# Performance work log

Hardware: AMD Instinct MI355X
Metric: run time of the kernel (lower is better)

Reference implementation:

```python
import jax, jax.numpy as jnp
import numpy as np

N_HEAD = 16
SIZE_PER_HEAD = 64
NEG_BIG = 1e12


def _len_mask(lengths, T):
    # Faithful to: mask = 1 - cumsum(one_hot(len, T), 1)
    # -> 1.0 for positions < len, 0.0 for positions >= len (all ones if len == T).
    pos = jnp.arange(T)
    return (pos[None, :] < lengths[:, 0, None]).astype(jnp.float32)  # [B, T]


def setup_inputs() -> dict:
    key = jax.random.key(0)
    ks = jax.random.split(key, 8)
    B, T, D = 2, 2048, 1024
    Q_seq = jax.random.normal(ks[0], (B, T, D), dtype=jnp.float32)
    K_seq = jax.random.normal(ks[1], (B, T, D), dtype=jnp.float32)
    V_seq = jax.random.normal(ks[2], (B, T, D), dtype=jnp.float32)
    Q_len = jax.random.randint(ks[3], (B, 1), 0, T, dtype=jnp.int32)
    V_len = jax.random.randint(ks[4], (B, 1), 0, T, dtype=jnp.int32)
    s = 1.0 / np.sqrt(D)
    WQ = jax.random.normal(ks[5], (D, N_HEAD * SIZE_PER_HEAD), dtype=jnp.float32) * s
    WK = jax.random.normal(ks[6], (D, N_HEAD * SIZE_PER_HEAD), dtype=jnp.float32) * s
    WV = jax.random.normal(ks[7], (D, N_HEAD * SIZE_PER_HEAD), dtype=jnp.float32) * s
    return {"Q_seq": Q_seq, "K_seq": K_seq, "V_seq": V_seq,
            "Q_len": Q_len, "V_len": V_len, "WQ": WQ, "WK": WK, "WV": WV}


def reference(Q_seq, K_seq, V_seq, Q_len, V_len, WQ, WK, WV):
    B, Tq, _ = Q_seq.shape
    Tk = K_seq.shape[1]
    H, dh = N_HEAD, SIZE_PER_HEAD

    q = (Q_seq @ WQ).reshape(B, Tq, H, dh)  # [B,Tq,H,dh]
    k = (K_seq @ WK).reshape(B, Tk, H, dh)
    v = (V_seq @ WV).reshape(B, Tk, H, dh)

    # scaled dot-product scores [B,H,Tq,Tk]
    A = jnp.einsum('bqhd,bkhd->bhqk', q, k) / np.sqrt(dh).astype(np.float32)

    # additive key-length mask over the key axis (original: permute+mask+permute)
    kmask = _len_mask(V_len, Tk)  # [B,Tk]
    A = A - (1.0 - kmask)[:, None, None, :] * NEG_BIG
    A = jax.nn.softmax(A, axis=-1)

    O = jnp.einsum('bhqk,bkhd->bqhd', A, v).reshape(B, Tq, H * dh)

    # multiplicative query-length mask
    qmask = _len_mask(Q_len, Tq)  # [B,Tq]
    return O * qmask[:, :, None]
```

## Files before the change

kernel.cpp:

```cpp
#include <hip/hip_runtime.h>


using short8   = __attribute__((ext_vector_type(8))) short;
using floatx4  = __attribute__((ext_vector_type(4))) float;
using floatx16 = __attribute__((ext_vector_type(16))) float;
using uintx4   = __attribute__((ext_vector_type(4))) unsigned int;
using ushort4v = __attribute__((ext_vector_type(4))) unsigned short;

__device__ __forceinline__ unsigned short f2bf(float f) {
    unsigned int u = __builtin_bit_cast(unsigned int, f);
    u += 0x7fffu + ((u >> 16) & 1u);
    return (unsigned short)(u >> 16);
}

__global__ __launch_bounds__(256) void cvt_kernel(
    const float* __restrict__ Qs, const float* __restrict__ Ks,
    const float* __restrict__ Vs, const int* __restrict__ Qlen,
    const int* __restrict__ Vlen, unsigned short* __restrict__ abf)
{
    int z = blockIdx.y, row = blockIdx.x;
    int b = row >> 11, rib = row & 2047;
    int ql = Qlen[b]; int vl = Vlen[b]; int vle = vl ? vl : 2048;
    int lim = (z == 0) ? ((ql + 127) & ~127) : ((vle + 127) & ~127);
    if (rib >= lim) return;
    const float* src = (z == 0) ? Qs : ((z == 1) ? Ks : Vs);
    int t = threadIdx.x;
    float4 v = *reinterpret_cast<const float4*>(src + (size_t)row * 1024 + t * 4);
    ushort4v o;
    o[0] = f2bf(v.x); o[1] = f2bf(v.y); o[2] = f2bf(v.z); o[3] = f2bf(v.w);
    *reinterpret_cast<ushort4v*>(abf + (size_t)z * 4194304u + (size_t)row * 1024 + t * 4) = o;
}

__global__ __launch_bounds__(256) void wt_kernel(
    const float* __restrict__ W0, const float* __restrict__ W1,
    const float* __restrict__ W2, unsigned short* __restrict__ out)
{
    __shared__ float tile[64][65];
    int z = blockIdx.z;
    const float* W = (z == 0) ? W0 : ((z == 1) ? W1 : W2);
    unsigned short* O = out + (size_t)z * 1048576u;
    int r0 = blockIdx.y * 64, c0 = blockIdx.x * 64;
    int t = threadIdx.x;
#pragma unroll
    for (int i = 0; i < 16; i++) {
        int idx = t + i * 256; int r = idx >> 6, c = idx & 63;
        tile[r][c] = W[(size_t)(r0 + r) * 1024 + c0 + c];
    }
    __syncthreads();
#pragma unroll
    for (int i = 0; i < 16; i++) {
        int idx = t + i * 256; int c = idx >> 6, r = idx & 63;
        O[(size_t)(c0 + c) * 1024 + r0 + r] = f2bf(tile[r][c]);
    }
}

template <bool PRECVT>
__global__ __launch_bounds__(256) void proj_kernel(
    const float* __restrict__ Qs, const float* __restrict__ Ks,
    const float* __restrict__ Vs, const unsigned short* __restrict__ abf,
    const unsigned short* __restrict__ wt,
    const int* __restrict__ Qlen, const int* __restrict__ Vlen,
    unsigned short* __restrict__ q, unsigned short* __restrict__ k,
    unsigned short* __restrict__ vT)
{
    __shared__ alignas(16) unsigned short As[128][72];
    __shared__ alignas(16) unsigned short Bs[128][72];

    int z = blockIdx.z;
    int tid = threadIdx.x;
    int m0 = blockIdx.y * 128, n0 = blockIdx.x * 128;
    int b = m0 >> 11, rib = m0 & 2047;
    int ql = Qlen[b]; int vl = Vlen[b]; int vle = vl ? vl : 2048;
    int lim = (z == 0) ? ((ql + 127) & ~127) : ((vle + 127) & ~127);
    if (rib >= lim) return;

    const float* Af = (z == 0) ? Qs : ((z == 1) ? Ks : Vs);
    const unsigned short* Ab = abf + (size_t)z * 4194304u;
    const unsigned short* Bt = wt + (size_t)z * 1048576u;

    int w = tid >> 6, lane = tid & 63, g = lane >> 4, lr = lane & 15;
    int wr = w >> 1, wc = w & 1;

    floatx4 acc[4][4];
#pragma unroll
    for (int m = 0; m < 4; m++)
#pragma unroll
        for (int n = 0; n < 4; n++) {
#pragma unroll
            for (int r = 0; r < 4; r++) acc[m][n][r] = 0.f;
        }

    int srow = tid >> 1, scol = (tid & 1) * 32;

    short8 pa[4], pb[4];
    float4 fa[8];

    if constexpr (PRECVT) {
#pragma unroll
        for (int i = 0; i < 4; i++)
            pa[i] = *reinterpret_cast<const short8*>(Ab + (size_t)(m0 + srow) * 1024 + scol + i * 8);
    } else {
#pragma unroll
        for (int i = 0; i < 8; i++)
            fa[i] = *reinterpret_cast<const float4*>(Af + (size_t)(m0 + srow) * 1024 + scol + i * 4);
    }
#pragma unroll
    for (int i = 0; i < 4; i++)
        pb[i] = *reinterpret_cast<const short8*>(Bt + (size_t)(n0 + srow) * 1024 + scol + i * 8);

    for (int kb = 0; kb < 1024; kb += 64) {
        __syncthreads();
        if constexpr (PRECVT) {
#pragma unroll
            for (int i = 0; i < 4; i++)
                *reinterpret_cast<short8*>(&As[srow][scol + i * 8]) = pa[i];
        } else {
#pragma unroll
            for (int i = 0; i < 4; i++) {
                short8 h;
                h[0] = (short)f2bf(fa[2*i].x);   h[1] = (short)f2bf(fa[2*i].y);
                h[2] = (short)f2bf(fa[2*i].z);   h[3] = (short)f2bf(fa[2*i].w);
                h[4] = (short)f2bf(fa[2*i+1].x); h[5] = (short)f2bf(fa[2*i+1].y);
                h[6] = (short)f2bf(fa[2*i+1].z); h[7] = (short)f2bf(fa[2*i+1].w);
                *reinterpret_cast<short8*>(&As[srow][scol + i * 8]) = h;
            }
        }
#pragma unroll
        for (int i = 0; i < 4; i++)
            *reinterpret_cast<short8*>(&Bs[srow][scol + i * 8]) = pb[i];
        __syncthreads();

        if (kb + 64 < 1024) {
            if constexpr (PRECVT) {
#pragma unroll
                for (int i = 0; i < 4; i++)
                    pa[i] = *reinterpret_cast<const short8*>(Ab + (size_t)(m0 + srow) * 1024 + kb + 64 + scol + i * 8);
            } else {
#pragma unroll
                for (int i = 0; i < 8; i++)
                    fa[i] = *reinterpret_cast<const float4*>(Af + (size_t)(m0 + srow) * 1024 + kb + 64 + scol + i * 4);
            }
#pragma unroll
            for (int i = 0; i < 4; i++)
                pb[i] = *reinterpret_cast<const short8*>(Bt + (size_t)(n0 + srow) * 1024 + kb + 64 + scol + i * 8);
        }

#pragma unroll
        for (int kc = 0; kc < 2; kc++) {
            short8 af[4], bf[4];
#pragma unroll
            for (int m = 0; m < 4; m++)
                af[m] = *reinterpret_cast<const short8*>(&As[wr * 64 + m * 16 + lr][kc * 32 + g * 8]);
#pragma unroll
            for (int n = 0; n < 4; n++)
                bf[n] = *reinterpret_cast<const short8*>(&Bs[wc * 64 + n * 16 + lr][kc * 32 + g * 8]);
#pragma unroll
            for (int m = 0; m < 4; m++)
#pragma unroll
                for (int n = 0; n < 4; n++)
                    acc[m][n] = __builtin_amdgcn_mfma_f32_16x16x32_bf16(af[m], bf[n], acc[m][n], 0, 0, 0);
        }
    }

    if (z < 2) {
        unsigned short* outp = (z == 0) ? q : k;
#pragma unroll
        for (int m = 0; m < 4; m++) {
            int row0 = m0 + wr * 64 + m * 16 + g * 4;
#pragma unroll
            for (int n = 0; n < 4; n++) {
                int col = n0 + wc * 64 + n * 16 + lr;
#pragma unroll
                for (int r = 0; r < 4; r++)
                    outp[(size_t)(row0 + r) * 1024 + col] = f2bf(acc[m][n][r]);
            }
        }
    } else {
#pragma unroll
        for (int m = 0; m < 4; m++) {
            int row0 = m0 + wr * 64 + m * 16 + g * 4;
            int bb = row0 >> 11, t0 = row0 & 2047;
#pragma unroll
            for (int n = 0; n < 4; n++) {
                int col = n0 + wc * 64 + n * 16 + lr;
                ushort4v pk;
#pragma unroll
                for (int r = 0; r < 4; r++) pk[r] = f2bf(acc[m][n][r]);
                *reinterpret_cast<ushort4v*>(vT + (size_t)(bb * 1024 + col) * 2048 + t0) = pk;
            }
        }
    }
}

__global__ __launch_bounds__(128, 2) void attn_kernel(
    const unsigned short* __restrict__ q, const unsigned short* __restrict__ k,
    const unsigned short* __restrict__ vT, const int* __restrict__ Qlen,
    const int* __restrict__ Vlen, float* __restrict__ out)
{
    __shared__ alignas(16) unsigned short ks[64][72];
    __shared__ alignas(16) unsigned short vs[64][72];

    int tid = threadIdx.x;
    int w = tid >> 6, lane = tid & 63;
    int j = lane & 31, hi = lane >> 5;

    int blk = blockIdx.x, xcd = blk & 7, idx = blk >> 3;
    int bh = xcd * 4 + (idx >> 5), qtile = idx & 31;
    int b = bh >> 4, h = bh & 15;
    int qlen = Qlen[b]; int vl = Vlen[b]; int vle = vl ? vl : 2048;
    int qrow0 = qtile * 64 + w * 32;

    if (qtile * 64 >= qlen) {
        int zr = qtile * 64 + (tid >> 1);
        float* p = out + (size_t)(b * 2048 + zr) * 1024 + h * 64 + (tid & 1) * 32;
        float4 z4; z4.x = 0.f; z4.y = 0.f; z4.z = 0.f; z4.w = 0.f;
#pragma unroll
        for (int s = 0; s < 8; s++) reinterpret_cast<float4*>(p)[s] = z4;
        return;
    }

    short8 qf[4];
    {
        const unsigned short* qp = q + (size_t)(b * 2048 + qrow0 + j) * 1024 + h * 64 + hi * 8;
#pragma unroll
        for (int c = 0; c < 4; c++) qf[c] = *reinterpret_cast<const short8*>(qp + c * 16);
    }

    floatx16 O0, O1;
#pragma unroll
    for (int t = 0; t < 16; t++) { O0[t] = 0.f; O1[t] = 0.f; }
    float m_r = -3.0e38f, l_r = 0.f;

    int nt = (vle + 63) >> 6;

    int srow = tid >> 1, scol = (tid & 1) * 32;
    const unsigned short* kg = k + (size_t)(b * 2048 + srow) * 1024 + h * 64 + scol;
    const unsigned short* vg = vT + (size_t)(b * 1024 + h * 64 + srow) * 2048 + scol;
    short8 pk[4], pv[4];
#pragma unroll
    for (int i = 0; i < 4; i++) {
        pk[i] = *reinterpret_cast<const short8*>(kg + i * 8);
        pv[i] = *reinterpret_cast<const short8*>(vg + i * 8);
    }

    const float CEXP = 0.18033688011112042f;

    for (int it = 0; it < nt; ++it) {
        int kt = it * 64;
        __syncthreads();
#pragma unroll
        for (int i = 0; i < 4; i++) {
            *reinterpret_cast<short8*>(&ks[srow][scol + i * 8]) = pk[i];
            *reinterpret_cast<short8*>(&vs[srow][scol + i * 8]) = pv[i];
        }
        __syncthreads();
        if (it + 1 < nt) {
            const unsigned short* kg2 = kg + (size_t)(kt + 64) * 1024;
            const unsigned short* vg2 = vg + (kt + 64);
#pragma unroll
            for (int i = 0; i < 4; i++) {
                pk[i] = *reinterpret_cast<const short8*>(kg2 + i * 8);
                pv[i] = *reinterpret_cast<const short8*>(vg2 + i * 8);
            }
        }

        floatx16 s0, s1;
#pragma unroll
        for (int t = 0; t < 16; t++) { s0[t] = 0.f; s1[t] = 0.f; }
        {
            short8 kf0[4], kf1[4];
#pragma unroll
            for (int c = 0; c < 4; c++) {
                kf0[c] = *reinterpret_cast<const short8*>(&ks[j][c * 16 + hi * 8]);
                kf1[c] = *reinterpret_cast<const short8*>(&ks[32 + j][c * 16 + hi * 8]);
            }
#pragma unroll
            for (int c = 0; c < 4; c++) {
                s0 = __builtin_amdgcn_mfma_f32_32x32x16_bf16(kf0[c], qf[c], s0, 0, 0, 0);
                s1 = __builtin_amdgcn_mfma_f32_32x32x16_bf16(kf1[c], qf[c], s1, 0, 0, 0);
            }
        }

        if (kt + 64 > vle) {
#pragma unroll
            for (int t = 0; t < 16; t++) {
                int kl = (t & 3) + 8 * (t >> 2) + 4 * hi;
                if (kt + kl >= vle)      s0[t] = -8.0e12f;
                if (kt + 32 + kl >= vle) s1[t] = -8.0e12f;
            }
        }

        float mx = s0[0];
#pragma unroll
        for (int t = 1; t < 16; t++) mx = fmaxf(mx, s0[t]);
#pragma unroll
        for (int t = 0; t < 16; t++) mx = fmaxf(mx, s1[t]);
        float lm = fmaxf(mx, __shfl_xor(mx, 32));

        if (__any(lm > m_r + 64.f)) {
            float mn = fmaxf(m_r, lm);
            float al = __builtin_amdgcn_exp2f((m_r - mn) * CEXP);
            m_r = mn;
            l_r *= al;
#pragma unroll
            for (int t = 0; t < 16; t++) { O0[t] *= al; O1[t] *= al; }
        }
        float nm = -m_r * CEXP;
#pragma unroll
        for (int t = 0; t < 16; t++) {
            s0[t] = __builtin_amdgcn_exp2f(fmaf(s0[t], CEXP, nm));
            s1[t] = __builtin_amdgcn_exp2f(fmaf(s1[t], CEXP, nm));
        }
        float rs = 0.f;
#pragma unroll
        for (int t = 0; t < 16; t++) rs += s0[t] + s1[t];
        l_r += rs;

        unsigned int pbw[4][4];
        {
            unsigned int D[4][2];
#pragma unroll
            for (int s = 0; s < 4; s++) {
                asm("v_cvt_pk_bf16_f32 %0, %1, %2" : "=v"(D[s][0]) : "v"(s0[4*s+0]), "v"(s0[4*s+1]));
                asm("v_cvt_pk_bf16_f32 %0, %1, %2" : "=v"(D[s][1]) : "v"(s0[4*s+2]), "v"(s0[4*s+3]));
            }
#pragma unroll
            for (int u = 0; u < 2; u++) {
                asm volatile("v_permlane32_swap_b32 %0, %1" : "+v"(D[0][u]), "+v"(D[1][u]));
                asm volatile("v_permlane32_swap_b32 %0, %1" : "+v"(D[2][u]), "+v"(D[3][u]));
                pbw[0][u] = D[0][u]; pbw[0][u + 2] = D[1][u];
                pbw[1][u] = D[2][u]; pbw[1][u + 2] = D[3][u];
            }
#pragma unroll
            for (int s = 0; s < 4; s++) {
                asm("v_cvt_pk_bf16_f32 %0, %1, %2" : "=v"(D[s][0]) : "v"(s1[4*s+0]), "v"(s1[4*s+1]));
                asm("v_cvt_pk_bf16_f32 %0, %1, %2" : "=v"(D[s][1]) : "v"(s1[4*s+2]), "v"(s1[4*s+3]));
            }
#pragma unroll
            for (int u = 0; u < 2; u++) {
                asm volatile("v_permlane32_swap_b32 %0, %1" : "+v"(D[0][u]), "+v"(D[1][u]));
                asm volatile("v_permlane32_swap_b32 %0, %1" : "+v"(D[2][u]), "+v"(D[3][u]));
                pbw[2][u] = D[0][u]; pbw[2][u + 2] = D[1][u];
                pbw[3][u] = D[2][u]; pbw[3][u + 2] = D[3][u];
            }
        }

        {
            short8 vf0[4], vf1[4];
#pragma unroll
            for (int c = 0; c < 4; c++) {
                vf0[c] = *reinterpret_cast<const short8*>(&vs[j][c * 16 + hi * 8]);
                vf1[c] = *reinterpret_cast<const short8*>(&vs[32 + j][c * 16 + hi * 8]);
            }
#pragma unroll
            for (int c = 0; c < 4; c++) {
                uintx4 pw; pw[0] = pbw[c][0]; pw[1] = pbw[c][1]; pw[2] = pbw[c][2]; pw[3] = pbw[c][3];
                short8 pf = __builtin_bit_cast(short8, pw);
                O0 = __builtin_amdgcn_mfma_f32_32x32x16_bf16(vf0[c], pf, O0, 0, 0, 0);
                O1 = __builtin_amdgcn_mfma_f32_32x32x16_bf16(vf1[c], pf, O1, 0, 0, 0);
            }
        }
    }

    float lt = l_r + __shfl_xor(l_r, 32);
    int qrow = qrow0 + j;
    float qm = (qrow < qlen) ? (1.0f / lt) : 0.f;
    float* ob = out + (size_t)(b * 2048 + qrow) * 1024 + h * 64;
#pragma unroll
    for (int s = 0; s < 4; s++) {
        float4 oa, obv;
        oa.x = O0[4*s+0] * qm; oa.y = O0[4*s+1] * qm; oa.z = O0[4*s+2] * qm; oa.w = O0[4*s+3] * qm;
        obv.x = O1[4*s+0] * qm; obv.y = O1[4*s+1] * qm; obv.z = O1[4*s+2] * qm; obv.w = O1[4*s+3] * qm;
        *reinterpret_cast<float4*>(ob + 8 * s + 4 * hi) = oa;
        *reinterpret_cast<float4*>(ob + 32 + 8 * s + 4 * hi) = obv;
    }
}

extern "C" void kernel_launch(void* const* d_in, const int* in_sizes, int n_in,
                              void* d_out, int out_size, void* d_ws, size_t ws_size,
                              hipStream_t stream)
{
    const float* Q_seq = (const float*)d_in[0];
    const float* K_seq = (const float*)d_in[1];
    const float* V_seq = (const float*)d_in[2];
    const int*   Q_len = (const int*)d_in[3];
    const int*   V_len = (const int*)d_in[4];
    const float* WQ    = (const float*)d_in[5];
    const float* WK    = (const float*)d_in[6];
    const float* WV    = (const float*)d_in[7];
    float* outp = (float*)d_out;

    unsigned short* wsb = (unsigned short*)d_ws;
    unsigned short* wt  = wsb;
    unsigned short* qp  = wsb + (size_t)3 * 1048576u;
    unsigned short* kp  = qp + 4194304u;
    unsigned short* vTp = kp + 4194304u;
    unsigned short* abf = vTp + 4194304u;

    size_t need = ((size_t)3 * 1048576u + 3u * 4194304u + (size_t)3 * 4194304u) * 2u;
    bool precvt = ws_size >= need;

    wt_kernel<<<dim3(16, 16, 3), 256, 0, stream>>>(WQ, WK, WV, wt);
    if (precvt) {
        cvt_kernel<<<dim3(4096, 3), 256, 0, stream>>>(Q_seq, K_seq, V_seq, Q_len, V_len, abf);
        proj_kernel<true><<<dim3(8, 32, 3), 256, 0, stream>>>(
            Q_seq, K_seq, V_seq, abf, wt, Q_len, V_len, qp, kp, vTp);
    } else {
        proj_kernel<false><<<dim3(8, 32, 3), 256, 0, stream>>>(
            Q_seq, K_seq, V_seq, nullptr, wt, Q_len, V_len, qp, kp, vTp);
    }
    attn_kernel<<<dim3(1024), 128, 0, stream>>>(qp, kp, vTp, Q_len, V_len, outp);
}
```

Before: 79.66 us.

## Split attention key range across four waves per query tile with LDS merge

Reworks the attention kernel so each 256-thread block handles 32 query rows, and its four waves each process an interleaved quarter of the key tiles (split-K flash attention). K and V fragments are loaded straight from global memory into registers instead of being staged through shared memory, which removes the per-iteration barriers. Partial max, sum and output are then merged through shared memory. This doubles the grid and raises parallelism for short sequences, at the cost of redundant global loads with no LDS reuse, no explicit prefetch, and a final reduction step.

```diff
diff --git a/kernel.cpp b/kernel.cpp
--- a/kernel.cpp
+++ b/kernel.cpp
@@ -192,30 +192,31 @@
     }
 }
 
-__global__ __launch_bounds__(128, 2) void attn_kernel(
+__global__ __launch_bounds__(256, 3) void attn_kernel(
     const unsigned short* __restrict__ q, const unsigned short* __restrict__ k,
     const unsigned short* __restrict__ vT, const int* __restrict__ Qlen,
     const int* __restrict__ Vlen, float* __restrict__ out)
 {
-    __shared__ alignas(16) unsigned short ks[64][72];
-    __shared__ alignas(16) unsigned short vs[64][72];
+    __shared__ float obuf[2][64][33];
+    __shared__ float mlbuf[4][2][33];
 
     int tid = threadIdx.x;
     int w = tid >> 6, lane = tid & 63;
     int j = lane & 31, hi = lane >> 5;
 
-    int blk = blockIdx.x, xcd = blk & 7, idx = blk >> 3;
-    int bh = xcd * 4 + (idx >> 5), qtile = idx & 31;
+    int blk = blockIdx.x;
+    int swz = (blk & 7) * 256 + (blk >> 3);
+    int bh = swz >> 6, qtile = swz & 63;
     int b = bh >> 4, h = bh & 15;
     int qlen = Qlen[b]; int vl = Vlen[b]; int vle = vl ? vl : 2048;
-    int qrow0 = qtile * 64 + w * 32;
-
-    if (qtile * 64 >= qlen) {
-        int zr = qtile * 64 + (tid >> 1);
-        float* p = out + (size_t)(b * 2048 + zr) * 1024 + h * 64 + (tid & 1) * 32;
+    int qrow0 = qtile * 32;
+
+    if (qrow0 >= qlen) {
+        int zr = qrow0 + (tid >> 3);
+        float* p = out + (size_t)(b * 2048 + zr) * 1024 + h * 64 + (tid & 7) * 8;
         float4 z4; z4.x = 0.f; z4.y = 0.f; z4.z = 0.f; z4.w = 0.f;
-#pragma unroll
-        for (int s = 0; s < 8; s++) reinterpret_cast<float4*>(p)[s] = z4;
+        *reinterpret_cast<float4*>(p) = z4;
+        *reinterpret_cast<float4*>(p + 4) = z4;
         return;
     }
 
@@ -232,53 +233,39 @@
     float m_r = -3.0e38f, l_r = 0.f;
 
     int nt = (vle + 63) >> 6;
-
-    int srow = tid >> 1, scol = (tid & 1) * 32;
-    const unsigned short* kg = k + (size_t)(b * 2048 + srow) * 1024 + h * 64 + scol;
-    const unsigned short* vg = vT + (size_t)(b * 1024 + h * 64 + srow) * 2048 + scol;
-    short8 pk[4], pv[4];
-#pragma unroll
-    for (int i = 0; i < 4; i++) {
-        pk[i] = *reinterpret_cast<const short8*>(kg + i * 8);
-        pv[i] = *reinterpret_cast<const short8*>(vg + i * 8);
-    }
+    int cnt = (nt > w) ? ((nt - w + 3) >> 2) : 0;
+
+    const unsigned short* kbase = k + (size_t)(b * 2048) * 1024 + h * 64 + hi * 8;
+    const unsigned short* vbase = vT + (size_t)(b * 1024 + h * 64 + j) * 2048 + hi * 8;
 
     const float CEXP = 0.18033688011112042f;
 
-    for (int it = 0; it < nt; ++it) {
-        int kt = it * 64;
-        __syncthreads();
-#pragma unroll
-        for (int i = 0; i < 4; i++) {
-            *reinterpret_cast<short8*>(&ks[srow][scol + i * 8]) = pk[i];
-            *reinterpret_cast<short8*>(&vs[srow][scol + i * 8]) = pv[i];
-        }
-        __syncthreads();
-        if (it + 1 < nt) {
-            const unsigned short* kg2 = kg + (size_t)(kt + 64) * 1024;
-            const unsigned short* vg2 = vg + (kt + 64);
-#pragma unroll
-            for (int i = 0; i < 4; i++) {
-                pk[i] = *reinterpret_cast<const short8*>(kg2 + i * 8);
-                pv[i] = *reinterpret_cast<const short8*>(vg2 + i * 8);
+    for (int i = 0; i < cnt; ++i) {
+        int kt = (w + 4 * i) << 6;
+
+        short8 kf0[4], kf1[4], vf0[4], vf1[4];
+        {
+            const unsigned short* kr0 = kbase + (size_t)(kt + j) * 1024;
+            const unsigned short* kr1 = kbase + (size_t)(kt + 32 + j) * 1024;
+#pragma unroll
+            for (int c = 0; c < 4; c++) {
+                kf0[c] = *reinterpret_cast<const short8*>(kr0 + c * 16);
+                kf1[c] = *reinterpret_cast<const short8*>(kr1 + c * 16);
+            }
+#pragma unroll
+            for (int c = 0; c < 4; c++) {
+                vf0[c] = *reinterpret_cast<const short8*>(vbase + kt + c * 16);
+                vf1[c] = *reinterpret_cast<const short8*>(vbase + 32 * 2048 + kt + c * 16);
             }
         }
 
         floatx16 s0, s1;
 #pragma unroll
         for (int t = 0; t < 16; t++) { s0[t] = 0.f; s1[t] = 0.f; }
-        {
-            short8 kf0[4], kf1[4];
-#pragma unroll
-            for (int c = 0; c < 4; c++) {
-                kf0[c] = *reinterpret_cast<const short8*>(&ks[j][c * 16 + hi * 8]);
-                kf1[c] = *reinterpret_cast<const short8*>(&ks[32 + j][c * 16 + hi * 8]);
-            }
-#pragma unroll
-            for (int c = 0; c < 4; c++) {
-                s0 = __builtin_amdgcn_mfma_f32_32x32x16_bf16(kf0[c], qf[c], s0, 0, 0, 0);
-                s1 = __builtin_amdgcn_mfma_f32_32x32x16_bf16(kf1[c], qf[c], s1, 0, 0, 0);
-            }
+#pragma unroll
+        for (int c = 0; c < 4; c++) {
+            s0 = __builtin_amdgcn_mfma_f32_32x32x16_bf16(kf0[c], qf[c], s0, 0, 0, 0);
+            s1 = __builtin_amdgcn_mfma_f32_32x32x16_bf16(kf1[c], qf[c], s1, 0, 0, 0);
         }
 
         if (kt + 64 > vle) {
@@ -345,34 +332,66 @@
             }
         }
 
-        {
-            short8 vf0[4], vf1[4];
-#pragma unroll
-            for (int c = 0; c < 4; c++) {
-                vf0[c] = *reinterpret_cast<const short8*>(&vs[j][c * 16 + hi * 8]);
-                vf1[c] = *reinterpret_cast<const short8*>(&vs[32 + j][c * 16 + hi * 8]);
-            }
-#pragma unroll
-            for (int c = 0; c < 4; c++) {
-                uintx4 pw; pw[0] = pbw[c][0]; pw[1] = pbw[c][1]; pw[2] = pbw[c][2]; pw[3] = pbw[c][3];
-                short8 pf = __builtin_bit_cast(short8, pw);
-                O0 = __builtin_amdgcn_mfma_f32_32x32x16_bf16(vf0[c], pf, O0, 0, 0, 0);
-                O1 = __builtin_amdgcn_mfma_f32_32x32x16_bf16(vf1[c], pf, O1, 0, 0, 0);
-            }
-        }
-    }
-
-    float lt = l_r + __shfl_xor(l_r, 32);
-    int qrow = qrow0 + j;
-    float qm = (qrow < qlen) ? (1.0f / lt) : 0.f;
-    float* ob = out + (size_t)(b * 2048 + qrow) * 1024 + h * 64;
-#pragma unroll
-    for (int s = 0; s < 4; s++) {
-        float4 oa, obv;
-        oa.x = O0[4*s+0] * qm; oa.y = O0[4*s+1] * qm; oa.z = O0[4*s+2] * qm; oa.w = O0[4*s+3] * qm;
-        obv.x = O1[4*s+0] * qm; obv.y = O1[4*s+1] * qm; obv.z = O1[4*s+2] * qm; obv.w = O1[4*s+3] * qm;
-        *reinterpret_cast<float4*>(ob + 8 * s + 4 * hi) = oa;
-        *reinterpret_cast<float4*>(ob + 32 + 8 * s + 4 * hi) = obv;
+#pragma unroll
+        for (int c = 0; c < 4; c++) {
+            uintx4 pw; pw[0] = pbw[c][0]; pw[1] = pbw[c][1]; pw[2] = pbw[c][2]; pw[3] = pbw[c][3];
+            short8 pf = __builtin_bit_cast(short8, pw);
+            O0 = __builtin_amdgcn_mfma_f32_32x32x16_bf16(vf0[c], pf, O0, 0, 0, 0);
+            O1 = __builtin_amdgcn_mfma_f32_32x32x16_bf16(vf1[c], pf, O1, 0, 0, 0);
+        }
+    }
+
+    l_r = l_r + __shfl_xor(l_r, 32);
+    if (hi == 0) mlbuf[w][0][j] = m_r;
+    __syncthreads();
+    float M = fmaxf(fmaxf(mlbuf[0][0][j], mlbuf[1][0][j]),
+                    fmaxf(mlbuf[2][0][j], mlbuf[3][0][j]));
+    float al = __builtin_amdgcn_exp2f((m_r - M) * CEXP);
+#pragma unroll
+    for (int t = 0; t < 16; t++) { O0[t] *= al; O1[t] *= al; }
+    if (hi == 0) mlbuf[w][1][j] = l_r * al;
+    if (w >= 2) {
+#pragma unroll
+        for (int t = 0; t < 16; t++) {
+            obuf[w - 2][lane][t]      = O0[t];
+            obuf[w - 2][lane][t + 16] = O1[t];
+        }
+    }
+    __syncthreads();
+    if (w < 2) {
+#pragma unroll
+        for (int t = 0; t < 16; t++) {
+            O0[t] += obuf[w][lane][t];
+            O1[t] += obuf[w][lane][t + 16];
+        }
+    }
+    __syncthreads();
+    if (w == 1) {
+#pragma unroll
+        for (int t = 0; t < 16; t++) {
+            obuf[0][lane][t]      = O0[t];
+            obuf[0][lane][t + 16] = O1[t];
+        }
+    }
+    __syncthreads();
+    if (w == 0) {
+#pragma unroll
+        for (int t = 0; t < 16; t++) {
+            O0[t] += obuf[0][lane][t];
+            O1[t] += obuf[0][lane][t + 16];
+        }
+        float lt = (mlbuf[0][1][j] + mlbuf[1][1][j]) + (mlbuf[2][1][j] + mlbuf[3][1][j]);
+        int qrow = qrow0 + j;
+        float qm = (qrow < qlen) ? (1.0f / lt) : 0.f;
+        float* ob = out + (size_t)(b * 2048 + qrow) * 1024 + h * 64;
+#pragma unroll
+        for (int s = 0; s < 4; s++) {
+            float4 oa, obv;
+            oa.x = O0[4*s+0] * qm; oa.y = O0[4*s+1] * qm; oa.z = O0[4*s+2] * qm; oa.w = O0[4*s+3] * qm;
+            obv.x = O1[4*s+0] * qm; obv.y = O1[4*s+1] * qm; obv.z = O1[4*s+2] * qm; obv.w = O1[4*s+3] * qm;
+            *reinterpret_cast<float4*>(ob + 8 * s + 4 * hi) = oa;
+            *reinterpret_cast<float4*>(ob + 32 + 8 * s + 4 * hi) = obv;
+        }
     }
 }
 
@@ -409,5 +428,5 @@
         proj_kernel<false><<<dim3(8, 32, 3), 256, 0, stream>>>(
             Q_seq, K_seq, V_seq, nullptr, wt, Q_len, V_len, qp, kp, vTp);
     }
-    attn_kernel<<<dim3(1024), 128, 0, stream>>>(qp, kp, vTp, Q_len, V_len, outp);
-}
+    attn_kernel<<<dim3(2048), 256, 0, stream>>>(qp, kp, vTp, Q_len, V_len, outp);
+}
```

Result: slower. 107.4 us (+34.8%).
